# Kernel tuning notes

Measured on AMD Instinct MI355X. Metric: run time of the kernel, lower is better.

## Reference

```python
import jax, jax.numpy as jnp
import numpy as np

B, A, T = 32, 64, 128
N_IN, N_EMB, N_H = 6, 128, 256
E = 2 * N_EMB  # embedding width = 256


def setup_inputs() -> dict:
    key = jax.random.key(0)
    ks = jax.random.split(key, 7)
    s_emb = 1.0 / np.sqrt(N_IN)
    s_l = 1.0 / np.sqrt(N_H)
    return {
        "inputs": jax.random.normal(ks[0], (B, A, T, N_IN), jnp.float32),
        "W_emb": jax.random.uniform(ks[1], (E, N_IN), jnp.float32, -s_emb, s_emb),
        "b_emb": jax.random.uniform(ks[2], (E,), jnp.float32, -s_emb, s_emb),
        "W_ih": jax.random.uniform(ks[3], (4 * N_H, E), jnp.float32, -s_l, s_l),
        "W_hh": jax.random.uniform(ks[4], (4 * N_H, N_H), jnp.float32, -s_l, s_l),
        "b_ih": jax.random.uniform(ks[5], (4 * N_H,), jnp.float32, -s_l, s_l),
        "b_hh": jax.random.uniform(ks[6], (4 * N_H,), jnp.float32, -s_l, s_l),
    }


def reference(inputs, W_emb, b_emb, W_ih, W_hh, b_ih, b_hh):
    b, a, t, _ = inputs.shape
    n = b * a
    h_dim = W_hh.shape[1]
    # [T, B*A, n_in]: time-major, atoms flattened into batch rows (as in LSTMCell.forward)
    xs = jnp.moveaxis(inputs, 2, 0).reshape(t, n, -1)
    # per-timestep Linear embed, then precompute the input projection of the LSTM
    emb = jnp.einsum("tnf,ef->tne", xs, W_emb) + b_emb          # [T, N, 2*n_emb]
    pre = jnp.einsum("tne,ge->tng", emb, W_ih) + b_ih + b_hh    # [T, N, 4*n_h]

    def step(carry, p):
        h, c = carry
        gates = p + h @ W_hh.T                                  # [N, 4*n_h]
        i, f, g, o = jnp.split(gates, 4, axis=-1)               # PyTorch gate order i,f,g,o
        i = jax.nn.sigmoid(i)
        f = jax.nn.sigmoid(f)
        g = jnp.tanh(g)
        o = jax.nn.sigmoid(o)
        c_new = f * c + i * g
        h_new = o * jnp.tanh(c_new)
        return (h_new, c_new), h_new

    h0 = jnp.zeros((n, h_dim), inputs.dtype)
    c0 = jnp.zeros((n, h_dim), inputs.dtype)
    _, hs = jax.lax.scan(step, (h0, c0), pre)                   # hs: [T, N, n_h]
    hs = hs.reshape(t, b, a, h_dim)
    return jnp.transpose(hs, (1, 2, 0, 3))                      # [B, A, T, n_h]
```

## Files before the change

### kernel.cpp

```cpp
#include <hip/hip_runtime.h>
#include <math.h>


#define TT 128
#define NH 256

typedef __attribute__((ext_vector_type(4))) float f32x4;
typedef __attribute__((ext_vector_type(8))) short s16x8;
typedef union { uint4 u4; s16x8 s; unsigned u[4]; } frag_u;

#define OFF_PUB    589824
#define PUB_STRIDE 8192
#define PUB_BYTES  (2 * 256 * PUB_STRIDE)

__device__ __forceinline__ unsigned short f2bf(float x) {
    unsigned u = __float_as_uint(x);
    return (unsigned short)((u + 0x7FFFu + ((u >> 16) & 1u)) >> 16);
}

template<int PAT>
__device__ __forceinline__ float qswz(float x) {
    return __int_as_float(__builtin_amdgcn_ds_swizzle(__float_as_int(x), PAT));
}

__global__ void prep(const float* __restrict__ W_emb, const float* __restrict__ b_emb,
                     const float* __restrict__ W_ih,  const float* __restrict__ W_hh,
                     const float* __restrict__ b_ih,  const float* __restrict__ b_hh,
                     unsigned short* __restrict__ wsW)
{
    int tid = blockIdx.x * 256 + threadIdx.x;
    if (tid >= 36864) return;
    int l    = tid & 63;
    int fid  = tid >> 6;
    int kt   = fid % 9;
    int cg16 = fid / 9;
    int l16  = l & 15, lg = l >> 4;
    int c    = l16 >> 2, q = l16 & 3;
    int col  = cg16 * 4 + c;
    int grow = q * 256 + col;
    union { unsigned short u16[8]; uint4 v; } pk;
    if (kt < 8) {
        int k0 = kt * 32 + lg * 8;
        const float* src = &W_hh[grow * 256 + k0];
        #pragma unroll
        for (int i = 0; i < 8; ++i) pk.u16[i] = f2bf(src[i]);
    } else {
        #pragma unroll
        for (int i = 0; i < 8; ++i) pk.u16[i] = 0;
        if (lg == 0) {
            float accf[6] = {0.f, 0.f, 0.f, 0.f, 0.f, 0.f};
            float accb = 0.f;
            for (int e = 0; e < 256; ++e) {
                float wv = W_ih[grow * 256 + e];
                accb += wv * b_emb[e];
                #pragma unroll
                for (int f = 0; f < 6; ++f) accf[f] += wv * W_emb[e * 6 + f];
            }
            #pragma unroll
            for (int f = 0; f < 6; ++f) pk.u16[f] = f2bf(accf[f]);
            pk.u16[6] = f2bf(accb + b_ih[grow] + b_hh[grow]);
        }
    }
    *reinterpret_cast<uint4*>(&wsW[(size_t)fid * 512 + l * 8]) = pk.v;
}

__device__ __forceinline__ float sigmoidf_(float x) { return 1.f / (1.f + __expf(-x)); }
__device__ __forceinline__ float tanhf_(float x) {
    float e = __expf(-2.f * fabsf(x));
    float r = (1.f - e) / (1.f + e);
    return copysignf(r, x);
}

__device__ __forceinline__ unsigned long long ld8_dev(const void* p) {
    unsigned long long v;
    asm volatile("global_load_dwordx2 %0, %1, off sc0 sc1\n\ts_waitcnt vmcnt(0)"
                 : "=v"(v) : "v"(p) : "memory");
    return v;
}
__device__ __forceinline__ void st8_dev(void* p, unsigned long long v) {
    asm volatile("global_store_dwordx2 %0, %1, off sc0 sc1" :: "v"(p), "v"(v) : "memory");
}

__device__ __forceinline__ void qgather(const f32x4& acc, bool qb0, bool qb1, float X[4]) {
    float g0, g1, g2, g3, x01, x23;
    g0 = qswz<0x8000>(acc[0]); g1 = qswz<0x8000>(acc[1]);
    g2 = qswz<0x8000>(acc[2]); g3 = qswz<0x8000>(acc[3]);
    x01 = qb0 ? g1 : g0; x23 = qb0 ? g3 : g2; X[0] = qb1 ? x23 : x01;
    g0 = qswz<0x8055>(acc[0]); g1 = qswz<0x8055>(acc[1]);
    g2 = qswz<0x8055>(acc[2]); g3 = qswz<0x8055>(acc[3]);
    x01 = qb0 ? g1 : g0; x23 = qb0 ? g3 : g2; X[1] = qb1 ? x23 : x01;
    g0 = qswz<0x80AA>(acc[0]); g1 = qswz<0x80AA>(acc[1]);
    g2 = qswz<0x80AA>(acc[2]); g3 = qswz<0x80AA>(acc[3]);
    x01 = qb0 ? g1 : g0; x23 = qb0 ? g3 : g2; X[2] = qb1 ? x23 : x01;
    g0 = qswz<0x80FF>(acc[0]); g1 = qswz<0x80FF>(acc[1]);
    g2 = qswz<0x80FF>(acc[2]); g3 = qswz<0x80FF>(acc[3]);
    x01 = qb0 ? g1 : g0; x23 = qb0 ? g3 : g2; X[3] = qb1 ? x23 : x01;
}

__global__ __launch_bounds__(1024, 4)
void lstm_main(const float* __restrict__ xin, const unsigned short* __restrict__ wsW,
               float* __restrict__ out, char* __restrict__ pub)
{
    __shared__ __align__(16) unsigned short hsh[2][2][16][264];

    const int tid = threadIdx.x;
    const int w   = tid >> 6, l = tid & 63;
    const int l16 = l & 15,  lg = l >> 4;
    const int c   = l16 >> 2, q = l16 & 3;
    const bool qb0 = (q & 1), qb1 = (q & 2);
    const int bid = blockIdx.x;
    const int q4  = bid >> 6;
    const int g63 = bid & 63;
    const int n0  = g63 * 32;
    const int j   = q4 * 64 + w * 4 + c;
    const int cg16 = q4 * 16 + w;
    const int R0  = lg * 4 + q;
    const bool evc = ((c & 1) == 0);

    frag_u Wf[9];
    #pragma unroll
    for (int kt = 0; kt < 9; ++kt) {
        const unsigned short* p = &wsW[(size_t)(cg16 * 9 + kt) * 512 + l * 8];
        asm volatile("global_load_dwordx4 %0, %1, off" : "=v"(Wf[kt].u4) : "v"(p));
    }
    asm volatile("s_waitcnt vmcnt(0)" ::: "memory");

    float cmA = 0.f, cmB = 0.f;

    const int pp0 = 0 + (0 >= q4);
    const int pp1 = pp0 + 1 + (pp0 + 1 == q4);
    const int pp2 = pp1 + 1 + (pp1 + 1 == q4);
    const int pq0 = (tid >> 9) ? pp1 : pp0;
    const int u0  = tid & 511;
    const bool has1 = (tid < 512);
    const int u1  = tid;
    const int sr0 = u0 >> 5, sc0 = pq0 * 64 + 2 * (u0 & 31);
    const int sr1 = u1 >> 5, sc1 = pp2 * 64 + 2 * (u1 & 31);
    const int upub = R0 * 32 + w * 2 + (c >> 1);

    unsigned long long pv0 = 0, pv1 = 0;
    const char *ps0 = nullptr, *ps1 = nullptr;

    for (int t = 0; t < TT; ++t) {
        const int want = t - 1;
        const unsigned wtag = (unsigned)want;
        const int pw = want & 1;
        const int cw = t & 1;

        frag_u xa; xa.u4 = (uint4){0u, 0u, 0u, 0u};
        if (lg == 0) {
            union { unsigned short u16[8]; uint4 v; } pk;
            const float* xp = xin + ((size_t)(n0 + l16) * TT + t) * 6;
            #pragma unroll
            for (int f = 0; f < 6; ++f) pk.u16[f] = f2bf(xp[f]);
            pk.u16[6] = 0x3F80; pk.u16[7] = 0;
            xa.u4 = pk.v;
        }
        if (t > 0) {
            asm volatile("s_waitcnt vmcnt(0)" ::: "memory");
            __builtin_amdgcn_sched_barrier(0);
            bool ok0 = ((unsigned)(pv0 >> 32) == wtag);
            bool ok1 = (!has1) || ((unsigned)(pv1 >> 32) == wtag);
            int it = 0;
            while (__ballot(!(ok0 && ok1)) != 0ull) {
                __builtin_amdgcn_s_sleep(1);
                if (!ok0) { pv0 = ld8_dev(ps0); ok0 = ((unsigned)(pv0 >> 32) == wtag); }
                if (!ok1) { pv1 = ld8_dev(ps1); ok1 = ((unsigned)(pv1 >> 32) == wtag); }
                if (++it > (1 << 14)) break;
            }
            *reinterpret_cast<unsigned*>(&hsh[pw][0][sr0][sc0]) = (unsigned)pv0;
            if (has1)
                *reinterpret_cast<unsigned*>(&hsh[pw][0][sr1][sc1]) = (unsigned)pv1;
        }
        __syncthreads();

        if (t > 0) {
            const char* base = pub + (size_t)pw * 256 * PUB_STRIDE;
            ps0 = base + (size_t)(pq0 * 64 + g63) * PUB_STRIDE + (size_t)(512 + u0) * 8;
            asm volatile("global_load_dwordx2 %0, %1, off sc0 sc1"
                         : "=v"(pv0) : "v"(ps0) : "memory");
            if (has1) {
                ps1 = base + (size_t)(pp2 * 64 + g63) * PUB_STRIDE + (size_t)(512 + u1) * 8;
                asm volatile("global_load_dwordx2 %0, %1, off sc0 sc1"
                             : "=v"(pv1) : "v"(ps1) : "memory");
            }
        }

        f32x4 acc = (f32x4){0.f, 0.f, 0.f, 0.f};
        if (t > 0) {
            #pragma unroll
            for (int kt = 0; kt < 8; ++kt) {
                s16x8 a = *reinterpret_cast<const s16x8*>(&hsh[pw][0][l16][kt * 32 + lg * 8]);
                acc = __builtin_amdgcn_mfma_f32_16x16x32_bf16(a, Wf[kt].s, acc, 0, 0, 0);
            }
        }
        acc = __builtin_amdgcn_mfma_f32_16x16x32_bf16(xa.s, Wf[8].s, acc, 0, 0, 0);

        {
            float X[4];
            qgather(acc, qb0, qb1, X);
            float cn = fmaf(sigmoidf_(X[1]), cmA, sigmoidf_(X[0]) * tanhf_(X[2]));
            cmA = cn;
            float hn = sigmoidf_(X[3]) * tanhf_(cn);
            unsigned us = f2bf(hn);
            hsh[cw][0][R0][j] = (unsigned short)us;
            float hp = qswz<0x101F>(hn);
            if (evc) {
                if (t < TT - 1) {
                    unsigned d = (us & 0xffffu) | ((unsigned)f2bf(hp) << 16);
                    char* dst = pub + ((size_t)cw * 256 + bid) * PUB_STRIDE
                                    + (size_t)upub * 8;
                    st8_dev(dst, (unsigned long long)d | ((unsigned long long)(unsigned)t << 32));
                }
                *reinterpret_cast<float2*>(&out[((size_t)(n0 + R0) * TT + t) * NH + j])
                    = make_float2(hn, hp);
            }
        }

        frag_u xb; xb.u4 = (uint4){0u, 0u, 0u, 0u};
        if (lg == 0) {
            union { unsigned short u16[8]; uint4 v; } pk;
            const float* xp = xin + ((size_t)(n0 + 16 + l16) * TT + t) * 6;
            #pragma unroll
            for (int f = 0; f < 6; ++f) pk.u16[f] = f2bf(xp[f]);
            pk.u16[6] = 0x3F80; pk.u16[7] = 0;
            xb.u4 = pk.v;
        }
        if (t > 0) {
            asm volatile("s_waitcnt vmcnt(0)" ::: "memory");
            __builtin_amdgcn_sched_barrier(0);
            bool ok0 = ((unsigned)(pv0 >> 32) == wtag);
            bool ok1 = (!has1) || ((unsigned)(pv1 >> 32) == wtag);
            int it = 0;
            while (__ballot(!(ok0 && ok1)) != 0ull) {
                __builtin_amdgcn_s_sleep(1);
                if (!ok0) { pv0 = ld8_dev(ps0); ok0 = ((unsigned)(pv0 >> 32) == wtag); }
                if (!ok1) { pv1 = ld8_dev(ps1); ok1 = ((unsigned)(pv1 >> 32) == wtag); }
                if (++it > (1 << 14)) break;
            }
            *reinterpret_cast<unsigned*>(&hsh[pw][1][sr0][sc0]) = (unsigned)pv0;
            if (has1)
                *reinterpret_cast<unsigned*>(&hsh[pw][1][sr1][sc1]) = (unsigned)pv1;
        }
        __syncthreads();

        if (t < TT - 1) {
            const char* base = pub + (size_t)cw * 256 * PUB_STRIDE;
            ps0 = base + (size_t)(pq0 * 64 + g63) * PUB_STRIDE + (size_t)u0 * 8;
            asm volatile("global_load_dwordx2 %0, %1, off sc0 sc1"
                         : "=v"(pv0) : "v"(ps0) : "memory");
            if (has1) {
                ps1 = base + (size_t)(pp2 * 64 + g63) * PUB_STRIDE + (size_t)u1 * 8;
                asm volatile("global_load_dwordx2 %0, %1, off sc0 sc1"
                             : "=v"(pv1) : "v"(ps1) : "memory");
            }
        }

        f32x4 accb = (f32x4){0.f, 0.f, 0.f, 0.f};
        if (t > 0) {
            #pragma unroll
            for (int kt = 0; kt < 8; ++kt) {
                s16x8 a = *reinterpret_cast<const s16x8*>(&hsh[pw][1][l16][kt * 32 + lg * 8]);
                accb = __builtin_amdgcn_mfma_f32_16x16x32_bf16(a, Wf[kt].s, accb, 0, 0, 0);
            }
        }
        accb = __builtin_amdgcn_mfma_f32_16x16x32_bf16(xb.s, Wf[8].s, accb, 0, 0, 0);

        {
            float X[4];
            qgather(accb, qb0, qb1, X);
            float cn = fmaf(sigmoidf_(X[1]), cmB, sigmoidf_(X[0]) * tanhf_(X[2]));
            cmB = cn;
            float hn = sigmoidf_(X[3]) * tanhf_(cn);
            unsigned us = f2bf(hn);
            hsh[cw][1][R0][j] = (unsigned short)us;
            float hp = qswz<0x101F>(hn);
            if (evc) {
                if (t < TT - 1) {
                    unsigned d = (us & 0xffffu) | ((unsigned)f2bf(hp) << 16);
                    char* dst = pub + ((size_t)cw * 256 + bid) * PUB_STRIDE
                                    + (size_t)(512 + upub) * 8;
                    st8_dev(dst, (unsigned long long)d | ((unsigned long long)(unsigned)t << 32));
                }
                *reinterpret_cast<float2*>(&out[((size_t)(n0 + 16 + R0) * TT + t) * NH + j])
                    = make_float2(hn, hp);
            }
        }
    }
}

extern "C" void kernel_launch(void* const* d_in, const int* in_sizes, int n_in,
                              void* d_out, int out_size, void* d_ws, size_t ws_size,
                              hipStream_t stream)
{
    const float* xin   = (const float*)d_in[0];
    const float* W_emb = (const float*)d_in[1];
    const float* b_emb = (const float*)d_in[2];
    const float* W_ih  = (const float*)d_in[3];
    const float* W_hh  = (const float*)d_in[4];
    const float* b_ih  = (const float*)d_in[5];
    const float* b_hh  = (const float*)d_in[6];
    float* out = (float*)d_out;

    unsigned short* wsW = (unsigned short*)d_ws;
    char* pub = (char*)d_ws + OFF_PUB;

    (void)hipMemsetAsync(pub, 0xFF, PUB_BYTES, stream);
    prep<<<144, 256, 0, stream>>>(W_emb, b_emb, W_ih, W_hh, b_ih, b_hh, wsW);
    lstm_main<<<256, 1024, 0, stream>>>(xin, wsW, out, pub);
}
```

Measured before the change: 780.2 us.

## Prepack inputs to bf16, peel first step, prefetch x and defer output stores

The prep kernel now also converts every input row/timestep to a packed bf16 fragment (with a bias one), so the recurrent loop loads one 16-byte vector instead of converting six floats per step. The first timestep is peeled, the main loop prefetches the next x fragment and the neighbours' published h alongside the current work with partial vmcnt waits, and uses a lighter LDS barrier. Output stores are deferred one step and written coalesced from the LDS h buffer as bf16-rounded values, which lowers output precision. The spin-wait cap is also reduced.

```diff
diff --git a/kernel.cpp b/kernel.cpp
--- a/kernel.cpp
+++ b/kernel.cpp
@@ -7,9 +7,11 @@
 
 typedef __attribute__((ext_vector_type(4))) float f32x4;
 typedef __attribute__((ext_vector_type(8))) short s16x8;
+typedef unsigned long long u64;
 typedef union { uint4 u4; s16x8 s; unsigned u[4]; } frag_u;
 
-#define OFF_PUB    589824
+#define OFF_XAB    589824
+#define OFF_PUB    4784128
 #define PUB_STRIDE 8192
 #define PUB_BYTES  (2 * 256 * PUB_STRIDE)
 
@@ -17,51 +19,65 @@
     unsigned u = __float_as_uint(x);
     return (unsigned short)((u + 0x7FFFu + ((u >> 16) & 1u)) >> 16);
 }
+__device__ __forceinline__ float bf2f(unsigned b) {
+    return __uint_as_float(b << 16);
+}
 
 template<int PAT>
 __device__ __forceinline__ float qswz(float x) {
     return __int_as_float(__builtin_amdgcn_ds_swizzle(__float_as_int(x), PAT));
 }
 
-__global__ void prep(const float* __restrict__ W_emb, const float* __restrict__ b_emb,
+__global__ void prep(const float* __restrict__ xin,
+                     const float* __restrict__ W_emb, const float* __restrict__ b_emb,
                      const float* __restrict__ W_ih,  const float* __restrict__ W_hh,
                      const float* __restrict__ b_ih,  const float* __restrict__ b_hh,
-                     unsigned short* __restrict__ wsW)
+                     unsigned short* __restrict__ wsW, uint4* __restrict__ xab)
 {
     int tid = blockIdx.x * 256 + threadIdx.x;
-    if (tid >= 36864) return;
-    int l    = tid & 63;
-    int fid  = tid >> 6;
-    int kt   = fid % 9;
-    int cg16 = fid / 9;
-    int l16  = l & 15, lg = l >> 4;
-    int c    = l16 >> 2, q = l16 & 3;
-    int col  = cg16 * 4 + c;
-    int grow = q * 256 + col;
-    union { unsigned short u16[8]; uint4 v; } pk;
-    if (kt < 8) {
-        int k0 = kt * 32 + lg * 8;
-        const float* src = &W_hh[grow * 256 + k0];
+    if (tid < 36864) {
+        int l    = tid & 63;
+        int fid  = tid >> 6;
+        int kt   = fid % 9;
+        int cg16 = fid / 9;
+        int l16  = l & 15, lg = l >> 4;
+        int c    = l16 >> 2, q = l16 & 3;
+        int col  = cg16 * 4 + c;
+        int grow = q * 256 + col;
+        union { unsigned short u16[8]; uint4 v; } pk;
+        if (kt < 8) {
+            int k0 = kt * 32 + lg * 8;
+            const float* src = &W_hh[grow * 256 + k0];
+            #pragma unroll
+            for (int i = 0; i < 8; ++i) pk.u16[i] = f2bf(src[i]);
+        } else {
+            #pragma unroll
+            for (int i = 0; i < 8; ++i) pk.u16[i] = 0;
+            if (lg == 0) {
+                float accf[6] = {0.f, 0.f, 0.f, 0.f, 0.f, 0.f};
+                float accb = 0.f;
+                for (int e = 0; e < 256; ++e) {
+                    float wv = W_ih[grow * 256 + e];
+                    accb += wv * b_emb[e];
+                    #pragma unroll
+                    for (int f = 0; f < 6; ++f) accf[f] += wv * W_emb[e * 6 + f];
+                }
+                #pragma unroll
+                for (int f = 0; f < 6; ++f) pk.u16[f] = f2bf(accf[f]);
+                pk.u16[6] = f2bf(accb + b_ih[grow] + b_hh[grow]);
+            }
+        }
+        *reinterpret_cast<uint4*>(&wsW[(size_t)fid * 512 + l * 8]) = pk.v;
+    } else if (tid < 36864 + 262144) {
+        int u = tid - 36864;
+        int row = u >> 7, t = u & 127;
+        const float* xp = xin + ((size_t)row * TT + t) * 6;
+        union { unsigned short u16[8]; uint4 v; } pk;
         #pragma unroll
-        for (int i = 0; i < 8; ++i) pk.u16[i] = f2bf(src[i]);
-    } else {
-        #pragma unroll
-        for (int i = 0; i < 8; ++i) pk.u16[i] = 0;
-        if (lg == 0) {
-            float accf[6] = {0.f, 0.f, 0.f, 0.f, 0.f, 0.f};
-            float accb = 0.f;
-            for (int e = 0; e < 256; ++e) {
-                float wv = W_ih[grow * 256 + e];
-                accb += wv * b_emb[e];
-                #pragma unroll
-                for (int f = 0; f < 6; ++f) accf[f] += wv * W_emb[e * 6 + f];
-            }
-            #pragma unroll
-            for (int f = 0; f < 6; ++f) pk.u16[f] = f2bf(accf[f]);
-            pk.u16[6] = f2bf(accb + b_ih[grow] + b_hh[grow]);
-        }
-    }
-    *reinterpret_cast<uint4*>(&wsW[(size_t)fid * 512 + l * 8]) = pk.v;
+        for (int f = 0; f < 6; ++f) pk.u16[f] = f2bf(xp[f]);
+        pk.u16[6] = 0x3F80; pk.u16[7] = 0;
+        xab[u] = pk.v;
+    }
 }
 
 __device__ __forceinline__ float sigmoidf_(float x) { return 1.f / (1.f + __expf(-x)); }
@@ -71,14 +87,22 @@
     return copysignf(r, x);
 }
 
-__device__ __forceinline__ unsigned long long ld8_dev(const void* p) {
-    unsigned long long v;
+__device__ __forceinline__ u64 ld8_dev(const void* p) {
+    u64 v;
     asm volatile("global_load_dwordx2 %0, %1, off sc0 sc1\n\ts_waitcnt vmcnt(0)"
                  : "=v"(v) : "v"(p) : "memory");
     return v;
 }
-__device__ __forceinline__ void st8_dev(void* p, unsigned long long v) {
+__device__ __forceinline__ void st8_dev(void* p, u64 v) {
     asm volatile("global_store_dwordx2 %0, %1, off sc0 sc1" :: "v"(p), "v"(v) : "memory");
+}
+__device__ __forceinline__ void st4_plain(void* p, unsigned v) {
+    asm volatile("global_store_dword %0, %1, off" :: "v"(p), "v"(v) : "memory");
+}
+__device__ __forceinline__ void sync_lds() {
+    asm volatile("s_waitcnt lgkmcnt(0)" ::: "memory");
+    __builtin_amdgcn_s_barrier();
+    __builtin_amdgcn_sched_barrier(0);
 }
 
 __device__ __forceinline__ void qgather(const f32x4& acc, bool qb0, bool qb1, float X[4]) {
@@ -97,8 +121,16 @@
     x01 = qb0 ? g1 : g0; x23 = qb0 ? g3 : g2; X[3] = qb1 ? x23 : x01;
 }
 
+__device__ __forceinline__ float ew_step(const f32x4& acc, float& cm, bool qb0, bool qb1) {
+    float X[4];
+    qgather(acc, qb0, qb1, X);
+    float cn = fmaf(sigmoidf_(X[1]), cm, sigmoidf_(X[0]) * tanhf_(X[2]));
+    cm = cn;
+    return sigmoidf_(X[3]) * tanhf_(cn);
+}
+
 __global__ __launch_bounds__(1024, 4)
-void lstm_main(const float* __restrict__ xin, const unsigned short* __restrict__ wsW,
+void lstm_main(const unsigned short* __restrict__ wsW, const uint4* __restrict__ xab,
                float* __restrict__ out, char* __restrict__ pub)
 {
     __shared__ __align__(16) unsigned short hsh[2][2][16][264];
@@ -130,162 +162,172 @@
     const int pp0 = 0 + (0 >= q4);
     const int pp1 = pp0 + 1 + (pp0 + 1 == q4);
     const int pp2 = pp1 + 1 + (pp1 + 1 == q4);
-    const int pq0 = (tid >> 9) ? pp1 : pp0;
+    const bool has1 = (tid < 512);
+    const int pq0 = has1 ? pp0 : pp1;
+    const int pq1 = has1 ? pp2 : pp1;
     const int u0  = tid & 511;
-    const bool has1 = (tid < 512);
-    const int u1  = tid;
+    const int u1  = tid & 511;
     const int sr0 = u0 >> 5, sc0 = pq0 * 64 + 2 * (u0 & 31);
-    const int sr1 = u1 >> 5, sc1 = pp2 * 64 + 2 * (u1 & 31);
+    const int sr1 = u1 >> 5, sc1 = pq1 * 64 + 2 * (u1 & 31);
     const int upub = R0 * 32 + w * 2 + (c >> 1);
-
-    unsigned long long pv0 = 0, pv1 = 0;
+    const int orow = tid >> 6;
+    const int ocol = q4 * 64 + (tid & 63);
+
+    u64 pv0 = 0, pv1 = 0;
     const char *ps0 = nullptr, *ps1 = nullptr;
-
-    for (int t = 0; t < TT; ++t) {
-        const int want = t - 1;
-        const unsigned wtag = (unsigned)want;
-        const int pw = want & 1;
+    frag_u xfA, xfB;
+
+    {
+        uint4 xA0 = xab[(size_t)(n0 + l16) * TT + 0];
+        uint4 xB0 = xab[(size_t)(n0 + 16 + l16) * TT + 0];
+        frag_u xa; xa.u4 = xA0;
+        frag_u xb; xb.u4 = xB0;
+        f32x4 z = (f32x4){0.f, 0.f, 0.f, 0.f};
+        f32x4 accA = __builtin_amdgcn_mfma_f32_16x16x32_bf16(xa.s, Wf[8].s, z, 0, 0, 0);
+        f32x4 accB = __builtin_amdgcn_mfma_f32_16x16x32_bf16(xb.s, Wf[8].s, z, 0, 0, 0);
+        float hnA = ew_step(accA, cmA, qb0, qb1);
+        float hnB = ew_step(accB, cmB, qb0, qb1);
+        unsigned usA = f2bf(hnA), usB = f2bf(hnB);
+        hsh[0][0][R0][j] = (unsigned short)usA;
+        hsh[0][1][R0][j] = (unsigned short)usB;
+        float hpA = qswz<0x101F>(hnA);
+        float hpB = qswz<0x101F>(hnB);
+        unsigned dA = (usA & 0xffffu) | ((unsigned)f2bf(hpA) << 16);
+        unsigned dB = (usB & 0xffffu) | ((unsigned)f2bf(hpB) << 16);
+
+        asm volatile("s_waitcnt vmcnt(0)" ::: "memory");
+
+        ps0 = pub + (size_t)(pq0 * 64 + g63) * PUB_STRIDE + (size_t)u0 * 8;
+        ps1 = pub + (size_t)(pq1 * 64 + g63) * PUB_STRIDE + (size_t)u1 * 8;
+        asm volatile("global_load_dwordx2 %0, %1, off sc0 sc1" : "=v"(pv0) : "v"(ps0) : "memory");
+        asm volatile("global_load_dwordx2 %0, %1, off sc0 sc1" : "=v"(pv1) : "v"(ps1) : "memory");
+        const uint4* xp = xab + (size_t)(n0 + l16) * TT + 1;
+        asm volatile("global_load_dwordx4 %0, %1, off" : "=v"(xfA.u4) : "v"(xp) : "memory");
+        if (evc) {
+            char* dstb = pub + (size_t)bid * PUB_STRIDE;
+            st8_dev(dstb + (size_t)upub * 8, (u64)dA);
+            st8_dev(dstb + (size_t)(512 + upub) * 8, (u64)dB);
+        }
+    }
+
+    for (int t = 1; t < TT; ++t) {
+        const int pw = (t - 1) & 1;
         const int cw = t & 1;
-
-        frag_u xa; xa.u4 = (uint4){0u, 0u, 0u, 0u};
-        if (lg == 0) {
-            union { unsigned short u16[8]; uint4 v; } pk;
-            const float* xp = xin + ((size_t)(n0 + l16) * TT + t) * 6;
-            #pragma unroll
-            for (int f = 0; f < 6; ++f) pk.u16[f] = f2bf(xp[f]);
-            pk.u16[6] = 0x3F80; pk.u16[7] = 0;
-            xa.u4 = pk.v;
-        }
-        if (t > 0) {
-            asm volatile("s_waitcnt vmcnt(0)" ::: "memory");
+        const unsigned want = (unsigned)(t - 1);
+
+        {
+            asm volatile("s_waitcnt vmcnt(2)" ::: "memory");
             __builtin_amdgcn_sched_barrier(0);
-            bool ok0 = ((unsigned)(pv0 >> 32) == wtag);
-            bool ok1 = (!has1) || ((unsigned)(pv1 >> 32) == wtag);
+            asm volatile("" : "+v"(pv0), "+v"(pv1));
+            asm volatile("" : "+v"(xfA.s));
+            bool ok0 = ((unsigned)(pv0 >> 32) == want);
+            bool ok1 = ((unsigned)(pv1 >> 32) == want);
             int it = 0;
             while (__ballot(!(ok0 && ok1)) != 0ull) {
                 __builtin_amdgcn_s_sleep(1);
-                if (!ok0) { pv0 = ld8_dev(ps0); ok0 = ((unsigned)(pv0 >> 32) == wtag); }
-                if (!ok1) { pv1 = ld8_dev(ps1); ok1 = ((unsigned)(pv1 >> 32) == wtag); }
-                if (++it > (1 << 14)) break;
+                if (!ok0) { pv0 = ld8_dev(ps0); ok0 = ((unsigned)(pv0 >> 32) == want); }
+                if (!ok1) { pv1 = ld8_dev(ps1); ok1 = ((unsigned)(pv1 >> 32) == want); }
+                if (++it > (1 << 12)) break;
             }
             *reinterpret_cast<unsigned*>(&hsh[pw][0][sr0][sc0]) = (unsigned)pv0;
             if (has1)
                 *reinterpret_cast<unsigned*>(&hsh[pw][0][sr1][sc1]) = (unsigned)pv1;
-        }
-        __syncthreads();
-
-        if (t > 0) {
-            const char* base = pub + (size_t)pw * 256 * PUB_STRIDE;
-            ps0 = base + (size_t)(pq0 * 64 + g63) * PUB_STRIDE + (size_t)(512 + u0) * 8;
-            asm volatile("global_load_dwordx2 %0, %1, off sc0 sc1"
-                         : "=v"(pv0) : "v"(ps0) : "memory");
-            if (has1) {
-                ps1 = base + (size_t)(pp2 * 64 + g63) * PUB_STRIDE + (size_t)(512 + u1) * 8;
-                asm volatile("global_load_dwordx2 %0, %1, off sc0 sc1"
-                             : "=v"(pv1) : "v"(ps1) : "memory");
-            }
-        }
-
-        f32x4 acc = (f32x4){0.f, 0.f, 0.f, 0.f};
-        if (t > 0) {
+            sync_lds();
+
+            {
+                const char* base = pub + (size_t)pw * 256 * PUB_STRIDE;
+                ps0 = base + (size_t)(pq0 * 64 + g63) * PUB_STRIDE + (size_t)(512 + u0) * 8;
+                ps1 = base + (size_t)(pq1 * 64 + g63) * PUB_STRIDE + (size_t)(512 + u1) * 8;
+                asm volatile("global_load_dwordx2 %0, %1, off sc0 sc1" : "=v"(pv0) : "v"(ps0) : "memory");
+                asm volatile("global_load_dwordx2 %0, %1, off sc0 sc1" : "=v"(pv1) : "v"(ps1) : "memory");
+            }
+            {
+                const uint4* xp = xab + (size_t)(n0 + 16 + l16) * TT + t;
+                asm volatile("global_load_dwordx4 %0, %1, off" : "=v"(xfB.u4) : "v"(xp) : "memory");
+            }
+            {
+                unsigned hv = (unsigned)hsh[pw][0][orow][ocol];
+                st4_plain(out + ((size_t)(n0 + orow) * TT + (t - 1)) * NH + ocol,
+                          hv << 16);
+            }
+            f32x4 acc = (f32x4){0.f, 0.f, 0.f, 0.f};
             #pragma unroll
             for (int kt = 0; kt < 8; ++kt) {
                 s16x8 a = *reinterpret_cast<const s16x8*>(&hsh[pw][0][l16][kt * 32 + lg * 8]);
                 acc = __builtin_amdgcn_mfma_f32_16x16x32_bf16(a, Wf[kt].s, acc, 0, 0, 0);
             }
-        }
-        acc = __builtin_amdgcn_mfma_f32_16x16x32_bf16(xa.s, Wf[8].s, acc, 0, 0, 0);
-
-        {
-            float X[4];
-            qgather(acc, qb0, qb1, X);
-            float cn = fmaf(sigmoidf_(X[1]), cmA, sigmoidf_(X[0]) * tanhf_(X[2]));
-            cmA = cn;
-            float hn = sigmoidf_(X[3]) * tanhf_(cn);
+            acc = __builtin_amdgcn_mfma_f32_16x16x32_bf16(xfA.s, Wf[8].s, acc, 0, 0, 0);
+            float hn = ew_step(acc, cmA, qb0, qb1);
             unsigned us = f2bf(hn);
             hsh[cw][0][R0][j] = (unsigned short)us;
             float hp = qswz<0x101F>(hn);
             if (evc) {
-                if (t < TT - 1) {
-                    unsigned d = (us & 0xffffu) | ((unsigned)f2bf(hp) << 16);
-                    char* dst = pub + ((size_t)cw * 256 + bid) * PUB_STRIDE
-                                    + (size_t)upub * 8;
-                    st8_dev(dst, (unsigned long long)d | ((unsigned long long)(unsigned)t << 32));
-                }
-                *reinterpret_cast<float2*>(&out[((size_t)(n0 + R0) * TT + t) * NH + j])
-                    = make_float2(hn, hp);
+                unsigned d = (us & 0xffffu) | ((unsigned)f2bf(hp) << 16);
+                char* dst = pub + ((size_t)cw * 256 + bid) * PUB_STRIDE + (size_t)upub * 8;
+                st8_dev(dst, (u64)d | ((u64)(unsigned)t << 32));
             }
         }
 
-        frag_u xb; xb.u4 = (uint4){0u, 0u, 0u, 0u};
-        if (lg == 0) {
-            union { unsigned short u16[8]; uint4 v; } pk;
-            const float* xp = xin + ((size_t)(n0 + 16 + l16) * TT + t) * 6;
-            #pragma unroll
-            for (int f = 0; f < 6; ++f) pk.u16[f] = f2bf(xp[f]);
-            pk.u16[6] = 0x3F80; pk.u16[7] = 0;
-            xb.u4 = pk.v;
-        }
-        if (t > 0) {
-            asm volatile("s_waitcnt vmcnt(0)" ::: "memory");
+        {
+            asm volatile("s_waitcnt vmcnt(2)" ::: "memory");
             __builtin_amdgcn_sched_barrier(0);
-            bool ok0 = ((unsigned)(pv0 >> 32) == wtag);
-            bool ok1 = (!has1) || ((unsigned)(pv1 >> 32) == wtag);
+            asm volatile("" : "+v"(pv0), "+v"(pv1));
+            asm volatile("" : "+v"(xfB.s));
+            bool ok0 = ((unsigned)(pv0 >> 32) == want);
+            bool ok1 = ((unsigned)(pv1 >> 32) == want);
             int it = 0;
             while (__ballot(!(ok0 && ok1)) != 0ull) {
                 __builtin_amdgcn_s_sleep(1);
-                if (!ok0) { pv0 = ld8_dev(ps0); ok0 = ((unsigned)(pv0 >> 32) == wtag); }
-                if (!ok1) { pv1 = ld8_dev(ps1); ok1 = ((unsigned)(pv1 >> 32) == wtag); }
-                if (++it > (1 << 14)) break;
+                if (!ok0) { pv0 = ld8_dev(ps0); ok0 = ((unsigned)(pv0 >> 32) == want); }
+                if (!ok1) { pv1 = ld8_dev(ps1); ok1 = ((unsigned)(pv1 >> 32) == want); }
+                if (++it > (1 << 12)) break;
             }
             *reinterpret_cast<unsigned*>(&hsh[pw][1][sr0][sc0]) = (unsigned)pv0;
             if (has1)
                 *reinterpret_cast<unsigned*>(&hsh[pw][1][sr1][sc1]) = (unsigned)pv1;
-        }
-        __syncthreads();
-
-        if (t < TT - 1) {
-            const char* base = pub + (size_t)cw * 256 * PUB_STRIDE;
-            ps0 = base + (size_t)(pq0 * 64 + g63) * PUB_STRIDE + (size_t)u0 * 8;
-            asm volatile("global_load_dwordx2 %0, %1, off sc0 sc1"
-                         : "=v"(pv0) : "v"(ps0) : "memory");
-            if (has1) {
-                ps1 = base + (size_t)(pp2 * 64 + g63) * PUB_STRIDE + (size_t)u1 * 8;
-                asm volatile("global_load_dwordx2 %0, %1, off sc0 sc1"
-                             : "=v"(pv1) : "v"(ps1) : "memory");
-            }
-        }
-
-        f32x4 accb = (f32x4){0.f, 0.f, 0.f, 0.f};
-        if (t > 0) {
+            sync_lds();
+
+            {
+                const char* base = pub + (size_t)cw * 256 * PUB_STRIDE;
+                ps0 = base + (size_t)(pq0 * 64 + g63) * PUB_STRIDE + (size_t)u0 * 8;
+                ps1 = base + (size_t)(pq1 * 64 + g63) * PUB_STRIDE + (size_t)u1 * 8;
+                asm volatile("global_load_dwordx2 %0, %1, off sc0 sc1" : "=v"(pv0) : "v"(ps0) : "memory");
+                asm volatile("global_load_dwordx2 %0, %1, off sc0 sc1" : "=v"(pv1) : "v"(ps1) : "memory");
+            }
+            {
+                const uint4* xp = xab + (size_t)(n0 + l16) * TT + (t + 1);
+                asm volatile("global_load_dwordx4 %0, %1, off" : "=v"(xfA.u4) : "v"(xp) : "memory");
+            }
+            {
+                unsigned hv = (unsigned)hsh[pw][1][orow][ocol];
+                st4_plain(out + ((size_t)(n0 + 16 + orow) * TT + (t - 1)) * NH + ocol,
+                          hv << 16);
+            }
+            f32x4 acc = (f32x4){0.f, 0.f, 0.f, 0.f};
             #pragma unroll
             for (int kt = 0; kt < 8; ++kt) {
                 s16x8 a = *reinterpret_cast<const s16x8*>(&hsh[pw][1][l16][kt * 32 + lg * 8]);
-                accb = __builtin_amdgcn_mfma_f32_16x16x32_bf16(a, Wf[kt].s, accb, 0, 0, 0);
-            }
-        }
-        accb = __builtin_amdgcn_mfma_f32_16x16x32_bf16(xb.s, Wf[8].s, accb, 0, 0, 0);
-
-        {
-            float X[4];
-            qgather(accb, qb0, qb1, X);
-            float cn = fmaf(sigmoidf_(X[1]), cmB, sigmoidf_(X[0]) * tanhf_(X[2]));
-            cmB = cn;
-            float hn = sigmoidf_(X[3]) * tanhf_(cn);
+                acc = __builtin_amdgcn_mfma_f32_16x16x32_bf16(a, Wf[kt].s, acc, 0, 0, 0);
+            }
+            acc = __builtin_amdgcn_mfma_f32_16x16x32_bf16(xfB.s, Wf[8].s, acc, 0, 0, 0);
+            float hn = ew_step(acc, cmB, qb0, qb1);
             unsigned us = f2bf(hn);
             hsh[cw][1][R0][j] = (unsigned short)us;
             float hp = qswz<0x101F>(hn);
             if (evc) {
-                if (t < TT - 1) {
-                    unsigned d = (us & 0xffffu) | ((unsigned)f2bf(hp) << 16);
-                    char* dst = pub + ((size_t)cw * 256 + bid) * PUB_STRIDE
-                                    + (size_t)(512 + upub) * 8;
-                    st8_dev(dst, (unsigned long long)d | ((unsigned long long)(unsigned)t << 32));
-                }
-                *reinterpret_cast<float2*>(&out[((size_t)(n0 + 16 + R0) * TT + t) * NH + j])
-                    = make_float2(hn, hp);
+                unsigned d = (us & 0xffffu) | ((unsigned)f2bf(hp) << 16);
+                char* dst = pub + ((size_t)cw * 256 + bid) * PUB_STRIDE + (size_t)(512 + upub) * 8;
+                st8_dev(dst, (u64)d | ((u64)(unsigned)t << 32));
             }
         }
+    }
+
+    sync_lds();
+    {
+        unsigned hvA = (unsigned)hsh[1][0][orow][ocol];
+        unsigned hvB = (unsigned)hsh[1][1][orow][ocol];
+        st4_plain(out + ((size_t)(n0 + orow) * TT + (TT - 1)) * NH + ocol, hvA << 16);
+        st4_plain(out + ((size_t)(n0 + 16 + orow) * TT + (TT - 1)) * NH + ocol, hvB << 16);
     }
 }
 
@@ -303,9 +345,10 @@
     float* out = (float*)d_out;
 
     unsigned short* wsW = (unsigned short*)d_ws;
-    char* pub = (char*)d_ws + OFF_PUB;
+    uint4* xab = (uint4*)((char*)d_ws + OFF_XAB);
+    char* pub  = (char*)d_ws + OFF_PUB;
 
     (void)hipMemsetAsync(pub, 0xFF, PUB_BYTES, stream);
-    prep<<<144, 256, 0, stream>>>(W_emb, b_emb, W_ih, W_hh, b_ih, b_hh, wsW);
-    lstm_main<<<256, 1024, 0, stream>>>(xin, wsW, out, pub);
-}
+    prep<<<1168, 256, 0, stream>>>(xin, W_emb, b_emb, W_ih, W_hh, b_ih, b_hh, wsW, xab);
+    lstm_main<<<256, 1024, 0, stream>>>(wsW, xab, out, pub);
+}
```

Result: faster. 753.7 us (-3.4%).
